# Kernel tuning notes

Measured on AMD Instinct MI355X. Metric: run time of the kernel, lower is better.

## Reference

```python
import jax, jax.numpy as jnp
import numpy as np

DIM = 512
NUM_HEADS = 8
DIM_HEAD = 64
EPS = 1e-8
ROPE_THETA = 10000.0


def rms_norm(x, gamma):
    # F.normalize(x, dim=-1, p=2, eps) * sqrt(dim) * gamma
    norm = jnp.sqrt(jnp.sum(x * x, axis=-1, keepdims=True))
    x = x / jnp.maximum(norm, EPS)
    return x * (DIM ** 0.5) * gamma


def apply_rope(x):
    # x: [b, h, n, d], interleaved-pair RoPE (rotary-embedding-torch style)
    n, d = x.shape[-2], x.shape[-1]
    inv_freq = 1.0 / (ROPE_THETA ** (jnp.arange(0, d, 2, dtype=jnp.float32) / d))
    freqs = jnp.arange(n, dtype=jnp.float32)[:, None] * inv_freq[None, :]  # [n, d/2]
    freqs = jnp.repeat(freqs, 2, axis=-1)  # [n, d]
    cos, sin = jnp.cos(freqs), jnp.sin(freqs)
    x1 = x[..., ::2]
    x2 = x[..., 1::2]
    rot = jnp.stack((-x2, x1), axis=-1).reshape(x.shape)
    return x * cos + rot * sin


def setup_inputs() -> dict:
    key = jax.random.key(0)
    k1, k2, k3, k4 = jax.random.split(key, 4)
    b, n = 4, 2048
    dim_inner = NUM_HEADS * DIM_HEAD
    x = jax.random.normal(k1, (b, n, DIM), dtype=jnp.float32)
    gamma = jnp.ones((DIM,), dtype=jnp.float32)
    w_qkv = jax.random.normal(k2, (DIM, 3 * dim_inner), dtype=jnp.float32) * (DIM ** -0.5)
    w_out = jax.random.normal(k3, (dim_inner, DIM), dtype=jnp.float32) * (dim_inner ** -0.5)
    return {"x": x, "gamma": gamma, "w_qkv": w_qkv, "w_out": w_out}


def reference(x, gamma, w_qkv, w_out):
    b, n, _ = x.shape
    h, d = NUM_HEADS, DIM_HEAD
    xn = rms_norm(x, gamma)
    qkv = xn @ w_qkv  # [b, n, 3*h*d]
    qkv = qkv.reshape(b, n, 3, h, d)
    q = jnp.transpose(qkv[:, :, 0], (0, 2, 1, 3))  # [b, h, n, d]
    k = jnp.transpose(qkv[:, :, 1], (0, 2, 1, 3))
    v = jnp.transpose(qkv[:, :, 2], (0, 2, 1, 3))
    q = apply_rope(q)
    k = apply_rope(k)
    scale = d ** -0.5
    attn = jnp.einsum('bhnd,bhmd->bhnm', q, k) * scale
    attn = jax.nn.softmax(attn, axis=-1)
    out = jnp.einsum('bhnm,bhmd->bhnd', attn, v)
    out = jnp.transpose(out, (0, 2, 1, 3)).reshape(b, n, h * d)
    return out @ w_out
```

## Files before the change

### kernel.cpp

```cpp
#include <hip/hip_runtime.h>
#include <hip/hip_bf16.h>
#include <cmath>

#define B_SZ 4
#define N_SEQ 2048
#define DIM 512
#define NH 8
#define DH 64
#define QKV_N 1536
#define ROWS (B_SZ * N_SEQ)

typedef __bf16 bf16x8 __attribute__((ext_vector_type(8)));
typedef __bf16 bf16x4 __attribute__((ext_vector_type(4)));
typedef float  f32x4  __attribute__((ext_vector_type(4)));

#define GLOAD_LDS16(gp, lp)                                                     \
    __builtin_amdgcn_global_load_lds(                                           \
        (const __attribute__((address_space(1))) void*)(gp),                    \
        (__attribute__((address_space(3))) void*)(lp), 16, 0, 0)

#define MFMA_BF16 __builtin_amdgcn_mfma_f32_16x16x32_bf16

#define SBAR() asm volatile("s_barrier" ::: "memory")

__device__ __forceinline__ void tcast_tile(const float* __restrict__ W,
                                           __bf16* __restrict__ Wt,
                                           int K, int N, int n0, int k0, int t,
                                           float (*Ls)[68]) {
    const int tx = t & 15, ty = t >> 4;
    #pragma unroll
    for (int i = 0; i < 4; i++) {
        int k = ty + i * 16;
        float4 v = *(const float4*)&W[(size_t)(k0 + k) * N + n0 + tx * 4];
        *(float4*)&Ls[k][tx * 4] = v;
    }
    __syncthreads();
    const int nrow = t >> 2, seg = (t & 3) * 16;
    bf16x8 o0, o1;
    #pragma unroll
    for (int j = 0; j < 8; j++) o0[j] = (__bf16)Ls[seg + j][nrow];
    #pragma unroll
    for (int j = 0; j < 8; j++) o1[j] = (__bf16)Ls[seg + 8 + j][nrow];
    *(bf16x8*)&Wt[(size_t)(n0 + nrow) * K + k0 + seg]     = o0;
    *(bf16x8*)&Wt[(size_t)(n0 + nrow) * K + k0 + seg + 8] = o1;
}

__global__ __launch_bounds__(256) void prelude_kernel(const float* __restrict__ x,
                                                      const float* __restrict__ gamma,
                                                      const float* __restrict__ w_qkv,
                                                      const float* __restrict__ w_out,
                                                      __bf16* __restrict__ A,
                                                      __bf16* __restrict__ Wqkvt,
                                                      __bf16* __restrict__ Woutt) {
    __shared__ float Ls[64][68];
    const int bx = blockIdx.x, t = threadIdx.x;
    if (bx < 2048) {
        const int row  = bx * 4 + (t >> 6);
        const int lane = t & 63;
        const float4* xr = (const float4*)(x + (size_t)row * DIM);
        float4 a = xr[lane];
        float4 b = xr[lane + 64];
        float ss = a.x*a.x + a.y*a.y + a.z*a.z + a.w*a.w
                 + b.x*b.x + b.y*b.y + b.z*b.z + b.w*b.w;
        #pragma unroll
        for (int off = 32; off > 0; off >>= 1) ss += __shfl_xor(ss, off, 64);
        float s = 22.62741699796952f / fmaxf(sqrtf(ss), 1e-8f);
        const float4* gr = (const float4*)gamma;
        float4 g1 = gr[lane], g2 = gr[lane + 64];
        bf16x4 o1 = { (__bf16)(a.x*g1.x*s), (__bf16)(a.y*g1.y*s),
                      (__bf16)(a.z*g1.z*s), (__bf16)(a.w*g1.w*s) };
        bf16x4 o2 = { (__bf16)(b.x*g2.x*s), (__bf16)(b.y*g2.y*s),
                      (__bf16)(b.z*g2.z*s), (__bf16)(b.w*g2.w*s) };
        *(bf16x4*)(A + (size_t)row * DIM + lane * 4)       = o1;
        *(bf16x4*)(A + (size_t)row * DIM + 256 + lane * 4) = o2;
    } else {
        const int idx = bx - 2048;
        const int k0 = (idx >> 5) * 64, c = idx & 31;
        if (c < 24) tcast_tile(w_qkv, Wqkvt, DIM, QKV_N, c * 64, k0, t, Ls);
        else        tcast_tile(w_out, Woutt, DIM, DIM, (c - 24) * 64, k0, t, Ls);
    }
}

__global__ __launch_bounds__(256) void gemm_qkv_kernel(const __bf16* __restrict__ A,
                                                       const __bf16* __restrict__ Bt,
                                                       __bf16* __restrict__ C,
                                                       __bf16* __restrict__ Vf) {
    __shared__ __bf16 As[3][128 * 32];
    __shared__ __bf16 Bs[3][128 * 32];
    const int t = threadIdx.x;
    const int lane = t & 63;
    const int w = t >> 6;
    const int l16 = lane & 15, quad = lane >> 4;
    const int wr = w >> 1, wc = w & 1;
    const int row0 = blockIdx.y * 128, col0 = blockIdx.x * 128;

    f32x4 acc[4][4] = {};

    const int r0a = t >> 2, ks0 = (t & 3) * 8;
    const int r1a = (t + 256) >> 2;

    auto dma = [&](int kidx, int bb) {
        const int kt = kidx * 32;
        GLOAD_LDS16(A  + (size_t)(row0 + r0a) * DIM + kt + ks0, As[bb] + t * 8);
        GLOAD_LDS16(A  + (size_t)(row0 + r1a) * DIM + kt + ks0, As[bb] + (t + 256) * 8);
        GLOAD_LDS16(Bt + (size_t)(col0 + r0a) * DIM + kt + ks0, Bs[bb] + t * 8);
        GLOAD_LDS16(Bt + (size_t)(col0 + r1a) * DIM + kt + ks0, Bs[bb] + (t + 256) * 8);
    };

    dma(0, 0);
    dma(1, 1);
    int cb = 0, wb = 2;
    for (int i = 0; i < 16; i++) {
        SBAR();
        if (i + 2 < 16) {
            dma(i + 2, wb);
            asm volatile("s_waitcnt vmcnt(8)" ::: "memory");
        } else if (i + 1 < 16) {
            asm volatile("s_waitcnt vmcnt(4)" ::: "memory");
        } else {
            asm volatile("s_waitcnt vmcnt(0)" ::: "memory");
        }
        SBAR();

        bf16x8 af[4], bfr[4];
        #pragma unroll
        for (int mi = 0; mi < 4; mi++)
            af[mi] = *(const bf16x8*)(As[cb] + (wr * 64 + mi * 16 + l16) * 32 + quad * 8);
        #pragma unroll
        for (int ni = 0; ni < 4; ni++)
            bfr[ni] = *(const bf16x8*)(Bs[cb] + (wc * 64 + ni * 16 + l16) * 32 + quad * 8);
        __builtin_amdgcn_s_setprio(1);
        #pragma unroll
        for (int mi = 0; mi < 4; mi++)
            #pragma unroll
            for (int ni = 0; ni < 4; ni++)
                acc[mi][ni] = MFMA_BF16(af[mi], bfr[ni], acc[mi][ni], 0, 0, 0);
        __builtin_amdgcn_s_setprio(0);
        cb = (cb == 2) ? 0 : cb + 1;
        wb = (wb == 2) ? 0 : wb + 1;
    }

    if (blockIdx.x >= 8) {
        const int head  = (blockIdx.x - 8) * 2 + wc;
        const int mbase = row0 + wr * 64;
        const int b     = mbase >> 11;
        const int nt    = (mbase >> 6) & 31;
        __bf16* vt = Vf + ((size_t)(b * 8 + head) * 32 + nt) * 4096;
        #pragma unroll
        for (int ni = 0; ni < 4; ni++)
            #pragma unroll
            for (int kc = 0; kc < 2; kc++) {
                bf16x8 o = { (__bf16)acc[2*kc][ni][0],   (__bf16)acc[2*kc][ni][1],
                             (__bf16)acc[2*kc][ni][2],   (__bf16)acc[2*kc][ni][3],
                             (__bf16)acc[2*kc+1][ni][0], (__bf16)acc[2*kc+1][ni][1],
                             (__bf16)acc[2*kc+1][ni][2], (__bf16)acc[2*kc+1][ni][3] };
                *(bf16x8*)(vt + (ni * 2 + kc) * 512 + lane * 8) = o;
            }
    } else {
        #pragma unroll
        for (int mi = 0; mi < 4; mi++)
            #pragma unroll
            for (int ni = 0; ni < 4; ni++)
                #pragma unroll
                for (int r = 0; r < 4; r++) {
                    int m = row0 + wr * 64 + mi * 16 + quad * 4 + r;
                    int n = col0 + wc * 64 + ni * 16 + l16;
                    C[(size_t)m * QKV_N + n] = (__bf16)acc[mi][ni][r];
                }
    }
}

__global__ __launch_bounds__(256) void gemm_out_kernel(const __bf16* __restrict__ A,
                                                       const __bf16* __restrict__ Bt,
                                                       float* __restrict__ C) {
    __shared__ __bf16 As[3][64 * 32];
    __shared__ __bf16 Bs[3][128 * 32];
    const int t = threadIdx.x;
    const int lane = t & 63;
    const int w = t >> 6;
    const int l16 = lane & 15, quad = lane >> 4;
    const int wr = w >> 1, wc = w & 1;
    const int row0 = blockIdx.y * 64, col0 = blockIdx.x * 128;

    f32x4 acc[2][4] = {};

    const int r0a = t >> 2, ks0 = (t & 3) * 8;
    const int r1a = (t + 256) >> 2;

    auto dma = [&](int kidx, int bb) {
        const int kt = kidx * 32;
        GLOAD_LDS16(A  + (size_t)(row0 + r0a) * DIM + kt + ks0, As[bb] + t * 8);
        GLOAD_LDS16(Bt + (size_t)(col0 + r0a) * DIM + kt + ks0, Bs[bb] + t * 8);
        GLOAD_LDS16(Bt + (size_t)(col0 + r1a) * DIM + kt + ks0, Bs[bb] + (t + 256) * 8);
    };

    dma(0, 0);
    dma(1, 1);
    int cb = 0, wb = 2;
    for (int i = 0; i < 16; i++) {
        SBAR();
        if (i + 2 < 16) {
            dma(i + 2, wb);
            asm volatile("s_waitcnt vmcnt(6)" ::: "memory");
        } else if (i + 1 < 16) {
            asm volatile("s_waitcnt vmcnt(3)" ::: "memory");
        } else {
            asm volatile("s_waitcnt vmcnt(0)" ::: "memory");
        }
        SBAR();

        bf16x8 af[2], bfr[4];
        #pragma unroll
        for (int mi = 0; mi < 2; mi++)
            af[mi] = *(const bf16x8*)(As[cb] + (wr * 32 + mi * 16 + l16) * 32 + quad * 8);
        #pragma unroll
        for (int ni = 0; ni < 4; ni++)
            bfr[ni] = *(const bf16x8*)(Bs[cb] + (wc * 64 + ni * 16 + l16) * 32 + quad * 8);
        __builtin_amdgcn_s_setprio(1);
        #pragma unroll
        for (int mi = 0; mi < 2; mi++)
            #pragma unroll
            for (int ni = 0; ni < 4; ni++)
                acc[mi][ni] = MFMA_BF16(af[mi], bfr[ni], acc[mi][ni], 0, 0, 0);
        __builtin_amdgcn_s_setprio(0);
        cb = (cb == 2) ? 0 : cb + 1;
        wb = (wb == 2) ? 0 : wb + 1;
    }
    #pragma unroll
    for (int mi = 0; mi < 2; mi++)
        #pragma unroll
        for (int ni = 0; ni < 4; ni++)
            #pragma unroll
            for (int r = 0; r < 4; r++) {
                int m = row0 + wr * 32 + mi * 16 + quad * 4 + r;
                int n = col0 + wc * 64 + ni * 16 + l16;
                C[(size_t)m * 512 + n] = acc[mi][ni][r];
            }
}

__global__ __launch_bounds__(256) void prep_kernel(const __bf16* __restrict__ qkvb,
                                                   __bf16* __restrict__ Qb,
                                                   __bf16* __restrict__ Kf) {
    const int bx = blockIdx.x;
    const int nt = bx & 31;
    const int bh = bx >> 5;
    const int b  = bh >> 3;
    const int h  = bh & 7;
    const int t  = threadIdx.x;
    const float QSCALE = 0.18033688011112042f;

    const int r  = t >> 2;
    const int d0 = (t & 3) << 4;
    const int pos = nt * 64 + r;
    const __bf16* qp = qkvb + (size_t)(b * N_SEQ + pos) * QKV_N + h * DH + d0;

    union Pack { __bf16 h[16]; uint4 u[2]; };
    Pack qi, ki, qo, ko;
    qi.u[0] = ((const uint4*)qp)[0];         qi.u[1] = ((const uint4*)qp)[1];
    ki.u[0] = ((const uint4*)(qp + 512))[0]; ki.u[1] = ((const uint4*)(qp + 512))[1];

    #pragma unroll
    for (int i = 0; i < 8; i++) {
        int p = (d0 >> 1) + i;
        float inv = exp2f(-0.41524101186092028f * (float)p);
        float ang = (float)pos * inv;
        float sn, cs;
        sincosf(ang, &sn, &cs);
        float qe = (float)qi.h[2*i], qd = (float)qi.h[2*i+1];
        float ke = (float)ki.h[2*i], kd = (float)ki.h[2*i+1];
        qo.h[2*i]   = (__bf16)(QSCALE * (qe * cs - qd * sn));
        qo.h[2*i+1] = (__bf16)(QSCALE * (qd * cs + qe * sn));
        ko.h[2*i]   = (__bf16)(ke * cs - kd * sn);
        ko.h[2*i+1] = (__bf16)(kd * cs + ke * sn);
    }
    uint4* qd_ = (uint4*)(Qb + ((size_t)bh * N_SEQ + pos) * DH + d0);
    qd_[0] = qo.u[0]; qd_[1] = qo.u[1];
    const int group = r >> 4, kl = r & 15;
    const int c = d0 >> 5, quad = (d0 & 31) >> 3;
    __bf16* kdst = Kf + ((size_t)bh * 32 + nt) * 4096
                      + (group * 2 + c) * 512 + (quad * 16 + kl) * 8;
    *(uint4*)kdst         = ko.u[0];
    *(uint4*)(kdst + 128) = ko.u[1];
}

__global__ __launch_bounds__(256, 2) void attn_mfma_kernel(const __bf16* __restrict__ Qb,
                                                           const __bf16* __restrict__ Kf,
                                                           const __bf16* __restrict__ Vf,
                                                           __bf16* __restrict__ attn) {
    __shared__ __bf16 kv[2][2][8192];

    const int t    = threadIdx.x;
    const int w    = t >> 6;
    const int lane = t & 63;
    const int l16  = lane & 15;
    const int quad = lane >> 4;
    const int qh   = w >> 1;
    const int kp   = w & 1;

    const int bx = blockIdx.x;
    const int bh = bx & 31;
    const int qc = bx >> 5;
    const int b  = bh >> 3;
    const int h  = bh & 7;

    const int qrow0 = qc * 128 + qh * 64;
    const __bf16* Qh = Qb + ((size_t)bh * N_SEQ + qrow0) * DH;
    const __bf16* Kt = Kf + (size_t)bh * 32 * 4096;
    const __bf16* Vt = Vf + (size_t)bh * 32 * 4096;

    bf16x8 qa[4][2];
    #pragma unroll
    for (int f = 0; f < 4; f++) {
        qa[f][0] = *(const bf16x8*)(Qh + (size_t)(f * 16 + l16) * DH + quad * 8);
        qa[f][1] = *(const bf16x8*)(Qh + (size_t)(f * 16 + l16) * DH + 32 + quad * 8);
    }

    bf16x8 ones;
    #pragma unroll
    for (int i = 0; i < 8; i++) ones[i] = (__bf16)1.0f;

    f32x4 O[4][4] = {};
    f32x4 L[4] = {};

    auto dma_tile = [&](int tidx, int p, int pp) {
        const __bf16* kss = Kt + (size_t)tidx * 4096;
        const __bf16* vss = Vt + (size_t)tidx * 4096;
        __bf16* dst = &kv[p][pp][0];
        GLOAD_LDS16(kss + t * 8,        dst + t * 8);
        GLOAD_LDS16(kss + 2048 + t * 8, dst + 2048 + t * 8);
        GLOAD_LDS16(vss + t * 8,        dst + 4096 + t * 8);
        GLOAD_LDS16(vss + 2048 + t * 8, dst + 4096 + 2048 + t * 8);
    };

    dma_tile(0, 0, 0);
    dma_tile(1, 1, 0);
    for (int i = 0; i < 16; i++) {
        const int cur = i & 1;
        SBAR();
        if (i + 1 < 16) {
            dma_tile(2 * (i + 1),     0, cur ^ 1);
            dma_tile(2 * (i + 1) + 1, 1, cur ^ 1);
            asm volatile("s_waitcnt vmcnt(8)" ::: "memory");
        } else {
            asm volatile("s_waitcnt vmcnt(0)" ::: "memory");
        }
        SBAR();

        const __bf16* kb = &kv[kp][cur][0];
        const __bf16* vb = &kv[kp][cur][4096];

        bf16x8 kf[4][2];
        #pragma unroll
        for (int g = 0; g < 4; g++)
            #pragma unroll
            for (int c = 0; c < 2; c++)
                kf[g][c] = *(const bf16x8*)(kb + (g * 2 + c) * 512 + lane * 8);

        bf16x8 pa[4][2];
        #pragma unroll
        for (int f = 0; f < 4; f++) {
            f32x4 S[4];
            __builtin_amdgcn_s_setprio(1);
            #pragma unroll
            for (int g = 0; g < 4; g++) {
                f32x4 z = {0, 0, 0, 0};
                z = MFMA_BF16(kf[g][0], qa[f][0], z, 0, 0, 0);
                z = MFMA_BF16(kf[g][1], qa[f][1], z, 0, 0, 0);
                S[g] = z;
            }
            __builtin_amdgcn_s_setprio(0);
            #pragma unroll
            for (int j = 0; j < 8; j++) {
                pa[f][0][j] = (__bf16)__builtin_amdgcn_exp2f(S[(j >> 2)][j & 3]);
                pa[f][1][j] = (__bf16)__builtin_amdgcn_exp2f(S[2 + (j >> 2)][j & 3]);
            }
        }

        bf16x8 vf[4][2];
        #pragma unroll
        for (int n = 0; n < 4; n++)
            #pragma unroll
            for (int kc = 0; kc < 2; kc++)
                vf[n][kc] = *(const bf16x8*)(vb + (n * 2 + kc) * 512 + lane * 8);

        __builtin_amdgcn_s_setprio(1);
        #pragma unroll
        for (int f = 0; f < 4; f++) {
            #pragma unroll
            for (int n = 0; n < 4; n++) {
                O[f][n] = MFMA_BF16(pa[f][0], vf[n][0], O[f][n], 0, 0, 0);
                O[f][n] = MFMA_BF16(pa[f][1], vf[n][1], O[f][n], 0, 0, 0);
            }
            L[f] = MFMA_BF16(pa[f][0], ones, L[f], 0, 0, 0);
            L[f] = MFMA_BF16(pa[f][1], ones, L[f], 0, 0, 0);
        }
        __builtin_amdgcn_s_setprio(0);
    }

    __syncthreads();
    float* reds = (float*)&kv[0][0][0];
    float* myO = reds + (size_t)(qh * 64 + lane) * 68;
    float* myL = reds + 128 * 68 + (size_t)(qh * 64 + lane) * 20;
    if (kp == 1) {
        #pragma unroll
        for (int f = 0; f < 4; f++) {
            #pragma unroll
            for (int n = 0; n < 4; n++)
                *(f32x4*)(myO + (f * 4 + n) * 4) = O[f][n];
            *(f32x4*)(myL + f * 4) = L[f];
        }
    }
    __syncthreads();
    if (kp == 0) {
        #pragma unroll
        for (int f = 0; f < 4; f++) {
            #pragma unroll
            for (int n = 0; n < 4; n++)
                O[f][n] += *(const f32x4*)(myO + (f * 4 + n) * 4);
            L[f] += *(const f32x4*)(myL + f * 4);
        }
        #pragma unroll
        for (int f = 0; f < 4; f++) {
            float inv[4];
            #pragma unroll
            for (int r = 0; r < 4; r++) inv[r] = 1.0f / L[f][r];
            #pragma unroll
            for (int n = 0; n < 4; n++)
                #pragma unroll
                for (int r = 0; r < 4; r++) {
                    size_t row = (size_t)(b * N_SEQ + qrow0 + f * 16 + quad * 4 + r);
                    attn[row * 512 + h * DH + n * 16 + l16] =
                        (__bf16)(O[f][n][r] * inv[r]);
                }
        }
    }
}

extern "C" void kernel_launch(void* const* d_in, const int* in_sizes, int n_in,
                              void* d_out, int out_size, void* d_ws, size_t ws_size,
                              hipStream_t stream) {
    const float* x     = (const float*)d_in[0];
    const float* gamma = (const float*)d_in[1];
    const float* w_qkv = (const float*)d_in[2];
    const float* w_out = (const float*)d_in[3];
    float* out = (float*)d_out;

    __bf16* Abf   = (__bf16*)d_ws;
    __bf16* Wqkvt = Abf + (size_t)ROWS * DIM;
    __bf16* Woutt = Wqkvt + (size_t)QKV_N * DIM;
    __bf16* qkvb  = Woutt + (size_t)DIM * DIM;
    __bf16* attnb = qkvb;
    __bf16* Qb    = qkvb + (size_t)ROWS * QKV_N;
    __bf16* Kf    = Qb + (size_t)NH * B_SZ * N_SEQ * DH;
    __bf16* Vf    = Kf + (size_t)NH * B_SZ * N_SEQ * DH;

    prelude_kernel<<<2304, 256, 0, stream>>>(x, gamma, w_qkv, w_out,
                                             Abf, Wqkvt, Woutt);
    gemm_qkv_kernel<<<dim3(QKV_N / 128, ROWS / 128), 256, 0, stream>>>(
        Abf, Wqkvt, qkvb, Vf);
    prep_kernel<<<1024, 256, 0, stream>>>(qkvb, Qb, Kf);
    attn_mfma_kernel<<<512, 256, 0, stream>>>(Qb, Kf, Vf, attnb);
    gemm_out_kernel<<<dim3(4, 128), 256, 0, stream>>>(attnb, Woutt, out);
}
```

Before: 152.0 us.

## Fuse RoPE and Q/K layout prep into QKV GEMM epilogue via LDS staging

Removes the separate prep kernel. The QKV GEMM epilogue now stages its output tile in LDS, applies RoPE and the Q scale there, and writes Q and K straight into their attention layouts. This drops a full round trip of the Q/K intermediate through global memory and one kernel launch. In exchange the GEMM epilogue gains extra LDS traffic, a barrier, and sincos math that could lengthen the tail of Q/K blocks.

```diff
diff --git a/kernel.cpp b/kernel.cpp
--- a/kernel.cpp
+++ b/kernel.cpp
@@ -83,10 +83,12 @@
 
 __global__ __launch_bounds__(256) void gemm_qkv_kernel(const __bf16* __restrict__ A,
                                                        const __bf16* __restrict__ Bt,
-                                                       __bf16* __restrict__ C,
+                                                       __bf16* __restrict__ Qb,
+                                                       __bf16* __restrict__ Kf,
                                                        __bf16* __restrict__ Vf) {
-    __shared__ __bf16 As[3][128 * 32];
-    __shared__ __bf16 Bs[3][128 * 32];
+    __shared__ __align__(16) __bf16 smem[24576];
+    __bf16* As = smem;
+    __bf16* Bs = smem + 12288;
     const int t = threadIdx.x;
     const int lane = t & 63;
     const int w = t >> 6;
@@ -101,10 +103,10 @@
 
     auto dma = [&](int kidx, int bb) {
         const int kt = kidx * 32;
-        GLOAD_LDS16(A  + (size_t)(row0 + r0a) * DIM + kt + ks0, As[bb] + t * 8);
-        GLOAD_LDS16(A  + (size_t)(row0 + r1a) * DIM + kt + ks0, As[bb] + (t + 256) * 8);
-        GLOAD_LDS16(Bt + (size_t)(col0 + r0a) * DIM + kt + ks0, Bs[bb] + t * 8);
-        GLOAD_LDS16(Bt + (size_t)(col0 + r1a) * DIM + kt + ks0, Bs[bb] + (t + 256) * 8);
+        GLOAD_LDS16(A  + (size_t)(row0 + r0a) * DIM + kt + ks0, As + bb * 4096 + t * 8);
+        GLOAD_LDS16(A  + (size_t)(row0 + r1a) * DIM + kt + ks0, As + bb * 4096 + (t + 256) * 8);
+        GLOAD_LDS16(Bt + (size_t)(col0 + r0a) * DIM + kt + ks0, Bs + bb * 4096 + t * 8);
+        GLOAD_LDS16(Bt + (size_t)(col0 + r1a) * DIM + kt + ks0, Bs + bb * 4096 + (t + 256) * 8);
     };
 
     dma(0, 0);
@@ -125,10 +127,10 @@
         bf16x8 af[4], bfr[4];
         #pragma unroll
         for (int mi = 0; mi < 4; mi++)
-            af[mi] = *(const bf16x8*)(As[cb] + (wr * 64 + mi * 16 + l16) * 32 + quad * 8);
+            af[mi] = *(const bf16x8*)(As + cb * 4096 + (wr * 64 + mi * 16 + l16) * 32 + quad * 8);
         #pragma unroll
         for (int ni = 0; ni < 4; ni++)
-            bfr[ni] = *(const bf16x8*)(Bs[cb] + (wc * 64 + ni * 16 + l16) * 32 + quad * 8);
+            bfr[ni] = *(const bf16x8*)(Bs + cb * 4096 + (wc * 64 + ni * 16 + l16) * 32 + quad * 8);
         __builtin_amdgcn_s_setprio(1);
         #pragma unroll
         for (int mi = 0; mi < 4; mi++)
@@ -156,17 +158,64 @@
                              (__bf16)acc[2*kc+1][ni][2], (__bf16)acc[2*kc+1][ni][3] };
                 *(bf16x8*)(vt + (ni * 2 + kc) * 512 + lane * 8) = o;
             }
-    } else {
-        #pragma unroll
-        for (int mi = 0; mi < 4; mi++)
-            #pragma unroll
-            for (int ni = 0; ni < 4; ni++)
-                #pragma unroll
-                for (int r = 0; r < 4; r++) {
-                    int m = row0 + wr * 64 + mi * 16 + quad * 4 + r;
-                    int n = col0 + wc * 64 + ni * 16 + l16;
-                    C[(size_t)m * QKV_N + n] = (__bf16)acc[mi][ni][r];
-                }
+        return;
+    }
+
+    __syncthreads();
+    __bf16* Ct = smem;
+    #pragma unroll
+    for (int mi = 0; mi < 4; mi++)
+        #pragma unroll
+        for (int ni = 0; ni < 4; ni++)
+            #pragma unroll
+            for (int r = 0; r < 4; r++)
+                Ct[(wr * 64 + mi * 16 + quad * 4 + r) * 136 + wc * 64 + ni * 16 + l16] =
+                    (__bf16)acc[mi][ni][r];
+    __syncthreads();
+
+    const bool  isQ   = (blockIdx.x < 4);
+    const float scale = isQ ? 0.18033688011112042f : 1.0f;
+    const int r  = t >> 2;
+    const int d0 = (t & 3) << 4;
+    const int b  = row0 >> 11;
+
+    union Pack { __bf16 h[16]; uint4 u[2]; };
+    #pragma unroll
+    for (int u = 0; u < 4; u++) {
+        const int ntsub = u >> 1, hs = u & 1;
+        const int nt  = ((row0 >> 6) & 31) + ntsub;
+        const int pos = ((row0 + ntsub * 64) & 2047) + r;
+        const int h   = (isQ ? blockIdx.x : blockIdx.x - 4) * 2 + hs;
+        const int bh  = b * 8 + h;
+
+        Pack vi, vo;
+        const __bf16* lp = Ct + (size_t)(ntsub * 64 + r) * 136 + hs * 64 + d0;
+        vi.u[0] = ((const uint4*)lp)[0];
+        vi.u[1] = ((const uint4*)lp)[1];
+
+        #pragma unroll
+        for (int i = 0; i < 8; i++) {
+            int p = (d0 >> 1) + i;
+            float inv = exp2f(-0.41524101186092028f * (float)p);
+            float ang = (float)pos * inv;
+            float sn, cs;
+            sincosf(ang, &sn, &cs);
+            float e = (float)vi.h[2*i], o = (float)vi.h[2*i+1];
+            vo.h[2*i]   = (__bf16)(scale * (e * cs - o * sn));
+            vo.h[2*i+1] = (__bf16)(scale * (o * cs + e * sn));
+        }
+
+        if (isQ) {
+            uint4* qd = (uint4*)(Qb + ((size_t)bh * N_SEQ + pos) * DH + d0);
+            qd[0] = vo.u[0]; qd[1] = vo.u[1];
+        } else {
+            const int group = r >> 4, kl = r & 15;
+            const int c = d0 >> 5, qd2 = (d0 & 31) >> 3;
+            __bf16* kdst = Kf + ((size_t)bh * 32 + nt) * 4096
+                              + (group * 2 + c) * 512 + (qd2 * 16 + kl) * 8;
+            *(uint4*)kdst         = vo.u[0];
+            *(uint4*)(kdst + 128) = vo.u[1];
+        }
     }
 }
 
@@ -238,51 +287,6 @@
             }
 }
 
-__global__ __launch_bounds__(256) void prep_kernel(const __bf16* __restrict__ qkvb,
-                                                   __bf16* __restrict__ Qb,
-                                                   __bf16* __restrict__ Kf) {
-    const int bx = blockIdx.x;
-    const int nt = bx & 31;
-    const int bh = bx >> 5;
-    const int b  = bh >> 3;
-    const int h  = bh & 7;
-    const int t  = threadIdx.x;
-    const float QSCALE = 0.18033688011112042f;
-
-    const int r  = t >> 2;
-    const int d0 = (t & 3) << 4;
-    const int pos = nt * 64 + r;
-    const __bf16* qp = qkvb + (size_t)(b * N_SEQ + pos) * QKV_N + h * DH + d0;
-
-    union Pack { __bf16 h[16]; uint4 u[2]; };
-    Pack qi, ki, qo, ko;
-    qi.u[0] = ((const uint4*)qp)[0];         qi.u[1] = ((const uint4*)qp)[1];
-    ki.u[0] = ((const uint4*)(qp + 512))[0]; ki.u[1] = ((const uint4*)(qp + 512))[1];
-
-    #pragma unroll
-    for (int i = 0; i < 8; i++) {
-        int p = (d0 >> 1) + i;
-        float inv = exp2f(-0.41524101186092028f * (float)p);
-        float ang = (float)pos * inv;
-        float sn, cs;
-        sincosf(ang, &sn, &cs);
-        float qe = (float)qi.h[2*i], qd = (float)qi.h[2*i+1];
-        float ke = (float)ki.h[2*i], kd = (float)ki.h[2*i+1];
-        qo.h[2*i]   = (__bf16)(QSCALE * (qe * cs - qd * sn));
-        qo.h[2*i+1] = (__bf16)(QSCALE * (qd * cs + qe * sn));
-        ko.h[2*i]   = (__bf16)(ke * cs - kd * sn);
-        ko.h[2*i+1] = (__bf16)(kd * cs + ke * sn);
-    }
-    uint4* qd_ = (uint4*)(Qb + ((size_t)bh * N_SEQ + pos) * DH + d0);
-    qd_[0] = qo.u[0]; qd_[1] = qo.u[1];
-    const int group = r >> 4, kl = r & 15;
-    const int c = d0 >> 5, quad = (d0 & 31) >> 3;
-    __bf16* kdst = Kf + ((size_t)bh * 32 + nt) * 4096
-                      + (group * 2 + c) * 512 + (quad * 16 + kl) * 8;
-    *(uint4*)kdst         = ko.u[0];
-    *(uint4*)(kdst + 128) = ko.u[1];
-}
-
 __global__ __launch_bounds__(256, 2) void attn_mfma_kernel(const __bf16* __restrict__ Qb,
                                                            const __bf16* __restrict__ Kf,
                                                            const __bf16* __restrict__ Vf,
@@ -448,17 +452,15 @@
     __bf16* Abf   = (__bf16*)d_ws;
     __bf16* Wqkvt = Abf + (size_t)ROWS * DIM;
     __bf16* Woutt = Wqkvt + (size_t)QKV_N * DIM;
-    __bf16* qkvb  = Woutt + (size_t)DIM * DIM;
-    __bf16* attnb = qkvb;
-    __bf16* Qb    = qkvb + (size_t)ROWS * QKV_N;
+    __bf16* attnb = Woutt + (size_t)DIM * DIM;
+    __bf16* Qb    = attnb + (size_t)ROWS * QKV_N;
     __bf16* Kf    = Qb + (size_t)NH * B_SZ * N_SEQ * DH;
     __bf16* Vf    = Kf + (size_t)NH * B_SZ * N_SEQ * DH;
 
     prelude_kernel<<<2304, 256, 0, stream>>>(x, gamma, w_qkv, w_out,
                                              Abf, Wqkvt, Woutt);
     gemm_qkv_kernel<<<dim3(QKV_N / 128, ROWS / 128), 256, 0, stream>>>(
-        Abf, Wqkvt, qkvb, Vf);
-    prep_kernel<<<1024, 256, 0, stream>>>(qkvb, Qb, Kf);
+        Abf, Wqkvt, Qb, Kf, Vf);
     attn_mfma_kernel<<<512, 256, 0, stream>>>(Qb, Kf, Vf, attnb);
     gemm_out_kernel<<<dim3(4, 128), 256, 0, stream>>>(attnb, Woutt, out);
 }
```

After: 150.8 us. About the same (-0.8%).
